# Optimization experiments

Measured on AMD Instinct MI355X. Metric: run time of the kernel, lower is better.

## Reference

```python
import jax, jax.numpy as jnp
import numpy as np

N_HEADS = 8
N_LAYERS = 2
LN_EPS = 1e-5


def _mha(x, Win, bin_, Wout, bout):
    # torch nn.MultiheadAttention, eval mode (dropout off). x: [b, s, d]
    b, s, d = x.shape
    dh = d // N_HEADS
    qkv = x @ Win.T + bin_                      # [b, s, 3d]
    q, k, v = jnp.split(qkv, 3, axis=-1)
    q = q.reshape(b, s, N_HEADS, dh)
    k = k.reshape(b, s, N_HEADS, dh)
    v = v.reshape(b, s, N_HEADS, dh)
    scores = jnp.einsum('bqhd,bkhd->bhqk', q, k) / jnp.sqrt(jnp.asarray(dh, x.dtype))
    attn = jax.nn.softmax(scores, axis=-1)
    o = jnp.einsum('bhqk,bkhd->bqhd', attn, v).reshape(b, s, d)
    return o @ Wout.T + bout


def _layer_norm(x, g, b):
    mu = jnp.mean(x, axis=-1, keepdims=True)
    var = jnp.mean(jnp.square(x - mu), axis=-1, keepdims=True)
    return (x - mu) * jax.lax.rsqrt(var + LN_EPS) * g + b


def _vertex_conv(feat, inc, prev, Win, bin_, Wout, bout, Wproj, ln_g, ln_b, alpha):
    # feat: [b,m,d], inc: [b,m,e]
    attn = _mha(feat, Win, bin_, Wout, bout)              # [b,m,d]
    scores = jnp.einsum('bme,bmd->bed', inc, attn)        # incidence aggregation
    w = jax.nn.softmax(scores, axis=1)                    # softmax over edges
    # fused form of einsum('bme,bmd->bmed') then einsum('bmed,bed->bed')
    edge = scores * w                                     # [b,e,d]
    edge = edge @ Wproj.T                                 # no-bias projection
    edge = _layer_norm(edge, ln_g, ln_b)
    if prev is not None:
        edge = alpha * prev + (1.0 - alpha) * edge
        edge = edge + prev
    return edge


def _edge_conv(inc, edge_feat, prev, Win, bin_, Wout, bout, Wproj, ln_g, ln_b, alpha):
    # inc: [b,m,e], edge_feat: [b,e,d]
    _ = _mha(edge_feat, Win, bin_, Wout, bout)            # attn computed, output unused downstream
    wef = jnp.einsum('bed,bme->bmd', edge_feat, inc)      # edge->node aggregation
    node = wef @ Wproj.T
    node = _layer_norm(node, ln_g, ln_b)
    if prev is not None:
        node = alpha * prev + (1.0 - alpha) * node
        node = node + prev
    return node


def setup_inputs() -> dict:
    key = jax.random.key(0)
    ks = jax.random.split(key, 8)
    b, m, e, d = 8, 1024, 1536, 256
    s = 0.02
    return {
        'features': jax.random.normal(ks[0], (b, m, d), jnp.float32),
        'inc_mat': (jax.random.uniform(ks[1], (b, m, e), jnp.float32) < 0.05).astype(jnp.float32),
        'vc_Win': jax.random.normal(ks[2], (3 * d, d), jnp.float32) * s,
        'vc_bin': jnp.zeros((3 * d,), jnp.float32),
        'vc_Wout': jax.random.normal(ks[3], (d, d), jnp.float32) * s,
        'vc_bout': jnp.zeros((d,), jnp.float32),
        'vc_Wproj': jax.random.normal(ks[4], (d, d), jnp.float32) * s,
        'vc_ln_g': jnp.ones((d,), jnp.float32),
        'vc_ln_b': jnp.zeros((d,), jnp.float32),
        'vc_alpha': jnp.asarray(0.5, jnp.float32),
        'ec_Win': jax.random.normal(ks[5], (3 * d, d), jnp.float32) * s,
        'ec_bin': jnp.zeros((3 * d,), jnp.float32),
        'ec_Wout': jax.random.normal(ks[6], (d, d), jnp.float32) * s,
        'ec_bout': jnp.zeros((d,), jnp.float32),
        'ec_Wproj': jax.random.normal(ks[7], (d, d), jnp.float32) * s,
        'ec_ln_g': jnp.ones((d,), jnp.float32),
        'ec_ln_b': jnp.zeros((d,), jnp.float32),
        'ec_alpha': jnp.asarray(0.5, jnp.float32),
    }


def reference(features, inc_mat,
              vc_Win, vc_bin, vc_Wout, vc_bout, vc_Wproj, vc_ln_g, vc_ln_b, vc_alpha,
              ec_Win, ec_bin, ec_Wout, ec_bout, ec_Wproj, ec_ln_g, ec_ln_b, ec_alpha):
    vc = (vc_Win, vc_bin, vc_Wout, vc_bout, vc_Wproj, vc_ln_g, vc_ln_b, vc_alpha)
    ec = (ec_Win, ec_bin, ec_Wout, ec_bout, ec_Wproj, ec_ln_g, ec_ln_b, ec_alpha)
    edge_feats = _vertex_conv(features, inc_mat, None, *vc)
    node_feats = _edge_conv(inc_mat, edge_feats, features, *ec)
    for _ in range(N_LAYERS):  # shared weights across layers, as in the torch module
        edge_feats = _vertex_conv(features, inc_mat, edge_feats, *vc)
        node_feats = _edge_conv(inc_mat, edge_feats, node_feats, *ec)
    return node_feats, edge_feats, inc_mat
```

## Files before the change

kernel.cpp:

```cpp
#include <hip/hip_runtime.h>
#include <stdint.h>


#define DEV static __device__ __forceinline__

typedef __attribute__((ext_vector_type(8))) short bf16x8;
typedef __attribute__((ext_vector_type(4))) float f32x4;

DEV uint16_t f2bf(float x){
  union{float f; uint32_t u;} v; v.f=x;
  uint32_t r = v.u + 0x7fffu + ((v.u>>16)&1u);
  return (uint16_t)(r>>16);
}
DEV float bf2f(uint16_t b){
  union{uint32_t u; float f;} v; v.u=((uint32_t)b)<<16; return v.f;
}

DEV uint32_t cvtpk_bf16(float lo, float hi){
  uint32_t d;
  asm("v_cvt_pk_bf16_f32 %0, %1, %2" : "=v"(d) : "v"(lo), "v"(hi));
  return d;
}

#if __has_builtin(__builtin_amdgcn_exp2f)
DEV float exp2fast(float x){ return __builtin_amdgcn_exp2f(x); }
#else
DEV float exp2fast(float x){ return __expf(x * 0.6931471805599453f); }
#endif

#if __has_builtin(__builtin_amdgcn_global_load_lds)
#define HAVE_GLL 1
#else
#define HAVE_GLL 0
#endif

DEV void load_lds16(const uint16_t* g, void* l){
#if HAVE_GLL
  __builtin_amdgcn_global_load_lds((const __attribute__((address_space(1))) uint32_t*)g,
                                   (__attribute__((address_space(3))) uint32_t*)l, 16, 0, 0);
#else
  *(bf16x8*)l = *(const bf16x8*)g;
#endif
}

__global__ __launch_bounds__(256)
void prep(const float* __restrict__ inc, float* __restrict__ out_inc,
          uint16_t* __restrict__ incb, uint16_t* __restrict__ incT,
          const float* __restrict__ feats, const float* __restrict__ win,
          const float* __restrict__ wout, const float* __restrict__ wpv,
          const float* __restrict__ wpe,
          uint16_t* __restrict__ xb, uint16_t* __restrict__ ow,
          uint16_t* __restrict__ oo, uint16_t* __restrict__ ov,
          uint16_t* __restrict__ oe){
  __shared__ float T[32][33];
  int bx = blockIdx.x;
  int tid = threadIdx.x;
  if (bx < 12288){
    int x = bx % 48;
    int t = bx / 48;
    int y = t % 32;
    int b = t / 32;
    int c0 = x*32, r0 = y*32;
    int tx = tid & 31, ty = tid >> 5;
    size_t base = (size_t)b*1024*1536;
#pragma unroll
    for (int j=0;j<4;++j){
      int r = r0 + ty + j*8;
      size_t idx = base + (size_t)r*1536 + c0 + tx;
      float v = inc[idx];
      T[ty+j*8][tx] = v;
      out_inc[idx] = v;
      incb[idx] = f2bf(v);
    }
    __syncthreads();
    size_t baseT = (size_t)b*1536*1024;
#pragma unroll
    for (int j=0;j<4;++j){
      int c = c0 + ty + j*8;
      incT[baseT + (size_t)c*1024 + r0 + tx] = f2bf(T[tx][ty+j*8]);
    }
  } else {
    int i = (bx - 12288)*256 + tid;
    const float* src; uint16_t* dst; int j;
    if (i < 524288){ src=feats; dst=xb; j=i; }
    else {
      i -= 524288;
      if (i < 49152){ src=win; dst=ow; j=i; }
      else if (i < 65536){ src=wout; dst=oo; j=i-49152; }
      else if (i < 81920){ src=wpv; dst=ov; j=i-65536; }
      else { src=wpe; dst=oe; j=i-81920; }
    }
    float4 v = ((const float4*)src)[j];
    union { uint16_t u[4]; uint64_t q; } p;
    p.u[0]=f2bf(v.x); p.u[1]=f2bf(v.y); p.u[2]=f2bf(v.z); p.u[3]=f2bf(v.w);
    ((uint64_t*)dst)[j] = p.q;
  }
}

template<int WM, int BK, int EPI>
__global__ __launch_bounds__(256, 3)
void gemm_nt(const uint16_t* __restrict__ A, const uint16_t* __restrict__ B,
             float* __restrict__ Cf, uint16_t* __restrict__ Cb,
             const float* __restrict__ bias,
             int M, int N, int K, long sA, long sB, long sC,
             float* __restrict__ extra){
  constexpr int AROWS = WM*32;
  constexpr int UPR = BK/8;
  constexpr int RPP = 256/UPR;
  __shared__ short As[AROWS*BK];
  __shared__ short Bs[128*BK];
  const int tid = threadIdx.x;
  const int lane = tid & 63;
  const int w = tid >> 6;
  const int wm = w & 1, wn = w >> 1;
  const int r = lane & 15, q = lane >> 4;
  const long zb = blockIdx.z;
  const uint16_t* Ab = A + zb*sA + (size_t)(blockIdx.x*AROWS)*K;
  const uint16_t* Bb = B + zb*sB + (size_t)(blockIdx.y*128)*K;
  f32x4 acc[WM][4];
#pragma unroll
  for (int i=0;i<WM;++i)
#pragma unroll
    for (int j=0;j<4;++j) acc[i][j] = (f32x4){0.f,0.f,0.f,0.f};

  const int srow = tid / UPR;
  const int sblk = tid % UPR;

  for (int kb = 0; kb < K; kb += BK){
#pragma unroll
    for (int i=0;i<AROWS/RPP;++i){
      int row = srow + RPP*i;
      int lblk = sblk ^ (row & (UPR-1));
      load_lds16(Ab + (size_t)row*K + kb + lblk*8, (char*)As + i*4096 + tid*16);
    }
#pragma unroll
    for (int i=0;i<128/RPP;++i){
      int row = srow + RPP*i;
      int lblk = sblk ^ (row & (UPR-1));
      load_lds16(Bb + (size_t)row*K + kb + lblk*8, (char*)Bs + i*4096 + tid*16);
    }
    __syncthreads();
#pragma unroll
    for (int kc=0;kc<BK/32;++kc){
      bf16x8 af[WM], bf[4];
#pragma unroll
      for (int mt=0;mt<WM;++mt){
        int m = wm*(WM*16) + mt*16 + r;
        af[mt] = *(const bf16x8*)&As[m*BK + ((kc*4 + q) ^ (m&(UPR-1)))*8];
      }
#pragma unroll
      for (int nt=0;nt<4;++nt){
        int n = wn*64 + nt*16 + r;
        bf[nt] = *(const bf16x8*)&Bs[n*BK + ((kc*4 + q) ^ (n&(UPR-1)))*8];
      }
#pragma unroll
      for (int mt=0;mt<WM;++mt)
#pragma unroll
        for (int nt=0;nt<4;++nt)
          acc[mt][nt] = __builtin_amdgcn_mfma_f32_16x16x32_bf16(af[mt], bf[nt], acc[mt][nt], 0,0,0);
    }
    __syncthreads();
  }

  const int gm0 = blockIdx.x*AROWS + wm*(WM*16);
  const int gn0 = blockIdx.y*128 + wn*64;

  if constexpr (EPI == 1){
#pragma unroll
    for (int mt=0;mt<WM;++mt){
      int gmb = gm0 + mt*16 + q*4;
      size_t bb_ = (size_t)(gmb>>10)*(256*1024);
      int mm = gmb & 1023;
#pragma unroll
      for (int nt=0;nt<4;++nt){
        int gn = gn0 + nt*16 + r;
        float bv = bias ? bias[gn] : 0.f;
        union{uint16_t u[4]; uint64_t q64;} pk;
#pragma unroll
        for (int reg=0;reg<4;++reg) pk.u[reg] = f2bf(acc[mt][nt][reg] + bv);
        *(uint64_t*)(Cb + bb_ + (size_t)gn*1024 + mm) = pk.q64;
      }
    }
  } else {
#pragma unroll
    for (int mt=0;mt<WM;++mt){
#pragma unroll
      for (int nt=0;nt<4;++nt){
        int gn = gn0 + nt*16 + r;
        float bv = bias ? bias[gn] : 0.f;
#pragma unroll
        for (int reg=0;reg<4;++reg){
          int gm = gm0 + mt*16 + q*4 + reg;
          float v = acc[mt][nt][reg] + bv;
          size_t off = (size_t)(zb*sC) + (size_t)gm*N + gn;
          if (Cf) Cf[off] = v;
          if (Cb) Cb[off] = f2bf(v);
        }
      }
    }
  }
  (void)extra;
}

__global__ __launch_bounds__(256, 4)
void gemm_score(const uint16_t* __restrict__ A,
                const uint16_t* __restrict__ B,
                float* __restrict__ part,
                uint16_t* __restrict__ VE){
  __shared__ short As[32*64];
  __shared__ short Bs[256*64];
  const int tid = threadIdx.x;
  const int lane = tid & 63;
  const int w = tid >> 6;
  const int r = lane & 15, q = lane >> 4;
  const int bx = (blockIdx.x & 7)*48 + (blockIdx.x >> 3);
  const int batch = bx / 48;
  const uint16_t* Ab = A + (size_t)bx*32*1024;
  const uint16_t* Bb = B + (size_t)batch*256*1024;

  f32x4 acc[2][4];
#pragma unroll
  for (int i=0;i<2;++i)
#pragma unroll
    for (int j=0;j<4;++j) acc[i][j] = (f32x4){0.f,0.f,0.f,0.f};

  const int srow = tid >> 3;
  const int sblk = tid & 7;

  for (int kb = 0; kb < 1024; kb += 64){
    { int lblk = sblk ^ (srow & 7);
      load_lds16(Ab + (size_t)srow*1024 + kb + lblk*8, (char*)As + tid*16); }
#pragma unroll
    for (int i=0;i<8;++i){
      int row = srow + 32*i;
      int lblk = sblk ^ (row & 7);
      load_lds16(Bb + (size_t)row*1024 + kb + lblk*8, (char*)Bs + i*4096 + tid*16);
    }
    __syncthreads();
#pragma unroll
    for (int kc=0;kc<2;++kc){
      bf16x8 af[2], bf[4];
#pragma unroll
      for (int mt=0;mt<2;++mt){
        int m = mt*16 + r;
        af[mt] = *(const bf16x8*)&As[m*64 + ((kc*4 + q) ^ (m&7))*8];
      }
#pragma unroll
      for (int nt=0;nt<4;++nt){
        int n = w*64 + nt*16 + r;
        bf[nt] = *(const bf16x8*)&Bs[n*64 + ((kc*4 + q) ^ (n&7))*8];
      }
#pragma unroll
      for (int mt=0;mt<2;++mt)
#pragma unroll
        for (int nt=0;nt<4;++nt)
          acc[mt][nt] = __builtin_amdgcn_mfma_f32_16x16x32_bf16(af[mt], bf[nt], acc[mt][nt], 0,0,0);
    }
    __syncthreads();
  }

#pragma unroll
  for (int nt=0;nt<4;++nt){
    int gn = w*64 + nt*16 + r;
    float s = 0.f;
#pragma unroll
    for (int mt=0;mt<2;++mt){
#pragma unroll
      for (int reg=0;reg<4;++reg){
        float v = acc[mt][nt][reg];
        float ev = __expf(v);
        s += ev;
        int row = mt*16 + q*4 + reg;
        VE[(size_t)(bx*32 + row)*256 + gn] = f2bf(v*ev);
      }
    }
    s += __shfl_xor(s, 16);
    s += __shfl_xor(s, 32);
    if (q == 0) part[(size_t)bx*256 + gn] = s;
  }
}

__global__ __launch_bounds__(256, 4)
void gemm_ln_edge(const uint16_t* __restrict__ SB, const uint16_t* __restrict__ B,
                  const float* __restrict__ part, const float* __restrict__ g,
                  const float* __restrict__ bb, const float* __restrict__ alpha,
                  float* __restrict__ out, uint16_t* __restrict__ baset){
  __shared__ short As[32*64];
  __shared__ short Bs[256*64];
  __shared__ float lnS[4][32], lnQ[4][32];
  __shared__ float PLinv[256];
  const int tid = threadIdx.x;
  const int lane = tid & 63;
  const int w = tid >> 6;
  const int r = lane & 15, q = lane >> 4;
  const int bx = (blockIdx.x & 7)*48 + (blockIdx.x >> 3);
  const int batch = bx / 48;

  {
    float s = 0.f;
#pragma unroll
    for (int i=0;i<48;++i) s += part[((size_t)batch*48 + i)*256 + tid];
    PLinv[tid] = 1.0f / s;
  }
  __syncthreads();

  f32x4 acc[2][4];
#pragma unroll
  for (int i=0;i<2;++i)
#pragma unroll
    for (int j=0;j<4;++j) acc[i][j] = (f32x4){0.f,0.f,0.f,0.f};

  const int srow = tid >> 3;
  const int sblk = tid & 7;

  for (int kb = 0; kb < 256; kb += 64){
    {
      bf16x8 v = *(const bf16x8*)(SB + (size_t)(bx*32 + srow)*256 + kb + sblk*8);
      const float* Lp = &PLinv[kb + sblk*8];
      float xv[8];
#pragma unroll
      for (int j=0;j<8;++j) xv[j] = bf2f((uint16_t)v[j]) * Lp[j];
      union{uint32_t u[4]; bf16x8 v8;} pk;
      pk.u[0] = cvtpk_bf16(xv[0], xv[1]);
      pk.u[1] = cvtpk_bf16(xv[2], xv[3]);
      pk.u[2] = cvtpk_bf16(xv[4], xv[5]);
      pk.u[3] = cvtpk_bf16(xv[6], xv[7]);
      *(bf16x8*)&As[srow*64 + (sblk ^ (srow&7))*8] = pk.v8;
    }
#pragma unroll
    for (int i=0;i<8;++i){
      int row = srow + 32*i;
      int lblk = sblk ^ (row & 7);
      load_lds16(B + (size_t)row*256 + kb + lblk*8, (char*)Bs + i*4096 + tid*16);
    }
    __syncthreads();
#pragma unroll
    for (int kc=0;kc<2;++kc){
      bf16x8 af[2], bf[4];
#pragma unroll
      for (int mt=0;mt<2;++mt){
        int m = mt*16 + r;
        af[mt] = *(const bf16x8*)&As[m*64 + ((kc*4 + q) ^ (m&7))*8];
      }
#pragma unroll
      for (int nt=0;nt<4;++nt){
        int n = w*64 + nt*16 + r;
        bf[nt] = *(const bf16x8*)&Bs[n*64 + ((kc*4 + q) ^ (n&7))*8];
      }
#pragma unroll
      for (int mt=0;mt<2;++mt)
#pragma unroll
        for (int nt=0;nt<4;++nt)
          acc[mt][nt] = __builtin_amdgcn_mfma_f32_16x16x32_bf16(af[mt], bf[nt], acc[mt][nt], 0,0,0);
    }
    __syncthreads();
  }

  float rs[2][4], rq[2][4];
#pragma unroll
  for (int mt=0;mt<2;++mt)
#pragma unroll
    for (int reg=0;reg<4;++reg){
      float s=0.f, s2=0.f;
#pragma unroll
      for (int nt=0;nt<4;++nt){
        float v = acc[mt][nt][reg];
        s += v; s2 += v*v;
      }
#pragma unroll
      for (int off=1; off<16; off<<=1){ s += __shfl_xor(s,off); s2 += __shfl_xor(s2,off); }
      rs[mt][reg]=s; rq[mt][reg]=s2;
    }
  if (r == 0){
#pragma unroll
    for (int mt=0;mt<2;++mt)
#pragma unroll
      for (int reg=0;reg<4;++reg){
        int row = mt*16 + q*4 + reg;
        lnS[w][row] = rs[mt][reg];
        lnQ[w][row] = rq[mt][reg];
      }
  }
  __syncthreads();

  const float c0 = 3.0f + alpha[0];
  float mu_[2][4], rstd_[2][4];
#pragma unroll
  for (int mt=0;mt<2;++mt)
#pragma unroll
    for (int reg=0;reg<4;++reg){
      int row = mt*16 + q*4 + reg;
      float S = lnS[0][row]+lnS[1][row]+lnS[2][row]+lnS[3][row];
      float Q = lnQ[0][row]+lnQ[1][row]+lnQ[2][row]+lnQ[3][row];
      float mu = S * (1.f/256.f);
      float var = fmaxf(Q*(1.f/256.f) - mu*mu, 0.f);
      mu_[mt][reg] = mu;
      rstd_[mt][reg] = rsqrtf(var + 1e-5f);
    }

  int e0 = (bx % 48) * 32;
#pragma unroll
  for (int mt=0;mt<2;++mt){
#pragma unroll
    for (int nt=0;nt<4;++nt){
      int gn = w*64 + nt*16 + r;
      float gv = g[gn], bv = bb[gn];
      union{uint16_t u[4]; uint64_t q64;} pk;
#pragma unroll
      for (int reg=0;reg<4;++reg){
        int row = mt*16 + q*4 + reg;
        size_t gm = (size_t)bx*32 + row;
        float o = ((acc[mt][nt][reg]-mu_[mt][reg])*rstd_[mt][reg]*gv + bv) * c0;
        pk.u[reg] = f2bf(o);
        out[gm*256 + gn] = o;
      }
      int ee = e0 + mt*16 + q*4;
      *(uint64_t*)(baset + ((size_t)batch*256 + gn)*1536 + ee) = pk.q64;
    }
  }
}

__global__ __launch_bounds__(256, 3)
void gemm_node_fused(const uint16_t* __restrict__ inc,
                     const uint16_t* __restrict__ baset,
                     const uint16_t* __restrict__ wpe,
                     const float* __restrict__ g, const float* __restrict__ bb,
                     const float* __restrict__ alpha,
                     const float* __restrict__ feats, float* __restrict__ out){
  __shared__ short Ws[256*64];
  __shared__ short As2[32*256];
  __shared__ short Is[32*64];
  const int tid = threadIdx.x;
  const int lane = tid & 63;
  const int w = tid >> 6;
  const int r = lane & 15, q = lane >> 4;
  const int bx = (blockIdx.x & 7)*32 + (blockIdx.x >> 3);
  const int batch = bx >> 5;
  const int mt0 = (bx & 31) * 32;

  const int srow = tid >> 3;
  const int sblk = tid & 7;

  const uint16_t* Bb = baset + (size_t)batch*256*1536;
  const uint16_t* Ib = inc + ((size_t)batch*1024 + mt0)*1536;

  f32x4 acc1[4][2];
#pragma unroll
  for (int i=0;i<4;++i)
#pragma unroll
    for (int j=0;j<2;++j) acc1[i][j] = (f32x4){0.f,0.f,0.f,0.f};

  for (int kb = 0; kb < 1536; kb += 64){
#pragma unroll
    for (int i=0;i<8;++i){
      int row = srow + 32*i;
      int lblk = sblk ^ (row & 7);
      load_lds16(Bb + (size_t)row*1536 + kb + lblk*8, (char*)Ws + i*4096 + tid*16);
    }
    { int lblk = sblk ^ (srow & 7);
      load_lds16(Ib + (size_t)srow*1536 + kb + lblk*8, (char*)Is + tid*16); }
    __syncthreads();
#pragma unroll
    for (int kc=0;kc<2;++kc){
      bf16x8 af[4], bf[2];
#pragma unroll
      for (int mt=0;mt<4;++mt){
        int d = w*64 + mt*16 + r;
        af[mt] = *(const bf16x8*)&Ws[d*64 + ((kc*4 + q) ^ (d&7))*8];
      }
#pragma unroll
      for (int nt=0;nt<2;++nt){
        int m = nt*16 + r;
        bf[nt] = *(const bf16x8*)&Is[m*64 + ((kc*4 + q) ^ (m&7))*8];
      }
#pragma unroll
      for (int mt=0;mt<4;++mt)
#pragma unroll
        for (int nt=0;nt<2;++nt)
          acc1[mt][nt] = __builtin_amdgcn_mfma_f32_16x16x32_bf16(af[mt], bf[nt], acc1[mt][nt], 0,0,0);
    }
    __syncthreads();
  }

#pragma unroll
  for (int mt=0;mt<4;++mt){
    int j = w*8 + mt*2 + (q>>1);
#pragma unroll
    for (int nt=0;nt<2;++nt){
      int m = nt*16 + r;
      union{uint16_t u[4]; uint64_t q64;} pk;
#pragma unroll
      for (int reg=0;reg<4;++reg) pk.u[reg] = f2bf(acc1[mt][nt][reg]);
      *(uint64_t*)((char*)As2 + m*512 + ((j ^ (m&7))<<4) + ((q&1)<<3)) = pk.q64;
    }
  }

  f32x4 acc2[4][2];
#pragma unroll
  for (int i=0;i<4;++i)
#pragma unroll
    for (int j=0;j<2;++j) acc2[i][j] = (f32x4){0.f,0.f,0.f,0.f};

  for (int kb = 0; kb < 256; kb += 64){
#pragma unroll
    for (int i=0;i<8;++i){
      int row = srow + 32*i;
      int lblk = sblk ^ (row & 7);
      load_lds16(wpe + (size_t)row*256 + kb + lblk*8, (char*)Ws + i*4096 + tid*16);
    }
    __syncthreads();
#pragma unroll
    for (int kc=0;kc<2;++kc){
      bf16x8 af[4], bf[2];
#pragma unroll
      for (int mt=0;mt<4;++mt){
        int dp = w*64 + mt*16 + r;
        af[mt] = *(const bf16x8*)&Ws[dp*64 + ((kc*4 + q) ^ (dp&7))*8];
      }
#pragma unroll
      for (int nt=0;nt<2;++nt){
        int m = nt*16 + r;
        int jr = (kb>>3) + kc*4 + q;
        bf[nt] = *(const bf16x8*)((char*)As2 + m*512 + ((jr ^ (m&7))<<4));
      }
#pragma unroll
      for (int mt=0;mt<4;++mt)
#pragma unroll
        for (int nt=0;nt<2;++nt)
          acc2[mt][nt] = __builtin_amdgcn_mfma_f32_16x16x32_bf16(af[mt], bf[nt], acc2[mt][nt], 0,0,0);
    }
    __syncthreads();
  }

  float* lnS = (float*)Is;
  float* lnQ = lnS + 128;
  float s_[2], q_[2];
#pragma unroll
  for (int nt=0;nt<2;++nt){
    float s=0.f, s2=0.f;
#pragma unroll
    for (int mt=0;mt<4;++mt)
#pragma unroll
      for (int reg=0;reg<4;++reg){
        float v = acc2[mt][nt][reg];
        s += v; s2 += v*v;
      }
    s += __shfl_xor(s,16); s2 += __shfl_xor(s2,16);
    s += __shfl_xor(s,32); s2 += __shfl_xor(s2,32);
    s_[nt]=s; q_[nt]=s2;
  }
  if (q == 0){
#pragma unroll
    for (int nt=0;nt<2;++nt){
      lnS[w*32 + nt*16 + r] = s_[nt];
      lnQ[w*32 + nt*16 + r] = q_[nt];
    }
  }
  __syncthreads();

  const float a = alpha[0];
  const float ap1 = 1.f + a;
  const float cn = (1.f - a)*(ap1*ap1 + ap1 + 1.f);
  const float cf = ap1*ap1*ap1;

  float mu_[2], rstd_[2];
#pragma unroll
  for (int nt=0;nt<2;++nt){
    int col = nt*16 + r;
    float S = lnS[col] + lnS[32+col] + lnS[64+col] + lnS[96+col];
    float Q = lnQ[col] + lnQ[32+col] + lnQ[64+col] + lnQ[96+col];
    float mu = S * (1.f/256.f);
    float var = fmaxf(Q*(1.f/256.f) - mu*mu, 0.f);
    mu_[nt] = mu;
    rstd_[nt] = rsqrtf(var + 1e-5f);
  }

#pragma unroll
  for (int mt=0;mt<4;++mt){
    int dp0 = w*64 + mt*16 + q*4;
    float4 gv = *(const float4*)&g[dp0];
    float4 bv = *(const float4*)&bb[dp0];
#pragma unroll
    for (int nt=0;nt<2;++nt){
      int m = nt*16 + r;
      size_t gm = (size_t)batch*1024 + mt0 + m;
      float4 fv = *(const float4*)&feats[gm*256 + dp0];
      float4 ov;
      ov.x = cf*fv.x + cn*((acc2[mt][nt][0]-mu_[nt])*rstd_[nt]*gv.x + bv.x);
      ov.y = cf*fv.y + cn*((acc2[mt][nt][1]-mu_[nt])*rstd_[nt]*gv.y + bv.y);
      ov.z = cf*fv.z + cn*((acc2[mt][nt][2]-mu_[nt])*rstd_[nt]*gv.z + bv.z);
      ov.w = cf*fv.w + cn*((acc2[mt][nt][3]-mu_[nt])*rstd_[nt]*gv.w + bv.w);
      *(float4*)&out[gm*256 + dp0] = ov;
    }
  }
}

DEV void stage_K(short* Kl, const uint16_t* __restrict__ qkv, size_t rowbase,
                 int c, int h, int kr){
  const uint16_t* kp = qkv + ((rowbase + c*256 + kr)*768 + 256 + h*32);
  int sz = (kr&3) ^ ((kr>>2)&1);
#pragma unroll
  for (int lb=0; lb<4; ++lb){
    bf16x8 v = *(const bf16x8*)(kp + lb*8);
    *(bf16x8*)&Kl[kr*32 + ((lb ^ sz))*8] = v;
  }
}

DEV void stage_V(short* VT, const uint16_t* __restrict__ qkv, size_t rowbase,
                 int c, int h, int t){
  int kvp = (t>>1)*2;
  int dhh = (t&1)*16;
  const uint16_t* v0 = qkv + ((rowbase + c*256 + kvp)*768 + 512 + h*32 + dhh);
  const uint16_t* v1 = v0 + 768;
  bf16x8 a0 = *(const bf16x8*)(v0);
  bf16x8 a1 = *(const bf16x8*)(v0+8);
  bf16x8 b0 = *(const bf16x8*)(v1);
  bf16x8 b1 = *(const bf16x8*)(v1+8);
  int blkbase = kvp>>3, off = kvp&7;
#pragma unroll
  for (int i=0;i<8;++i){
    int dh = dhh + i;
    uint32_t pack = (uint32_t)(uint16_t)a0[i] | ((uint32_t)(uint16_t)b0[i]<<16);
    *(uint32_t*)&VT[dh*256 + ((blkbase ^ (dh&7))*8) + off] = pack;
  }
#pragma unroll
  for (int i=0;i<8;++i){
    int dh = dhh + 8 + i;
    uint32_t pack = (uint32_t)(uint16_t)a1[i] | ((uint32_t)(uint16_t)b1[i]<<16);
    *(uint32_t*)&VT[dh*256 + ((blkbase ^ (dh&7))*8) + off] = pack;
  }
}

__global__ __launch_bounds__(512)
void attn_fwd(const uint16_t* __restrict__ qkv, uint16_t* __restrict__ O){
  __shared__ short Kl[256*32];
  __shared__ short VT[32*256];
  __shared__ short Pl[8][16*36];
  const int tid = threadIdx.x, lane = tid&63, w = tid>>6;
  const int r = lane&15, q = lane>>4;
  const int logical = (blockIdx.x & 7)*64 + (blockIdx.x >> 3);
  const int bh = logical >> 3, qc = logical & 7;
  const int b = bh>>3, h = bh&7;
  const int q0 = qc*128 + w*16;
  const size_t rowbase = (size_t)b*1024;

  bf16x8 aq;
  {
    const float qscale = 0.25505654380651023f;
    const uint16_t* p = qkv + ((rowbase + q0 + r)*768 + h*32 + q*8);
    bf16x8 t = *(const bf16x8*)p;
#pragma unroll
    for (int j=0;j<8;++j)
      t[j] = (short)f2bf(bf2f((uint16_t)t[j]) * qscale);
    aq = t;
  }

  f32x4 o[2];
  o[0]=(f32x4){0.f,0.f,0.f,0.f}; o[1]=(f32x4){0.f,0.f,0.f,0.f};
  float l = 0.f;

  for (int c=0;c<4;++c){
    __syncthreads();
    if (tid < 256) stage_K(Kl, qkv, rowbase, c, h, tid);
    else           stage_V(VT, qkv, rowbase, c, h, tid-256);
    __syncthreads();
    for (int s32=0; s32<8; ++s32){
#pragma unroll
      for (int t2=0;t2<2;++t2){
        int rn = s32*32 + t2*16 + r;
        int sz = (rn&3) ^ ((rn>>2)&1);
        bf16x8 bk = *(const bf16x8*)&Kl[rn*32 + ((q ^ sz))*8];
        f32x4 z = (f32x4){0.f,0.f,0.f,0.f};
        f32x4 st = __builtin_amdgcn_mfma_f32_16x16x32_bf16(bk, aq, z, 0,0,0);
        float p0 = exp2fast(st[0]);
        float p1 = exp2fast(st[1]);
        float p2 = exp2fast(st[2]);
        float p3 = exp2fast(st[3]);
        l += (p0+p1)+(p2+p3);
        union{uint32_t u[2]; uint64_t q64;} pk;
        pk.u[0] = cvtpk_bf16(p0, p1);
        pk.u[1] = cvtpk_bf16(p2, p3);
        *(uint64_t*)&Pl[w][r*36 + t2*16 + q*4] = pk.q64;
      }
      bf16x8 bv[2];
#pragma unroll
      for (int db=0;db<2;++db){
        int dh = db*16 + r;
        bv[db] = *(const bf16x8*)&VT[dh*256 + (((s32*4 + q) ^ (dh&7)))*8];
      }
      bf16x8 ap = *(const bf16x8*)&Pl[w][r*36 + q*8];
#pragma unroll
      for (int db=0;db<2;++db)
        o[db] = __builtin_amdgcn_mfma_f32_16x16x32_bf16(ap, bv[db], o[db], 0,0,0);
    }
  }

  l += __shfl_xor(l, 16);
  l += __shfl_xor(l, 32);
#pragma unroll
  for (int db=0;db<2;++db)
#pragma unroll
    for (int reg=0;reg<4;++reg){
      float li = __shfl(l, q*4 + reg);
      int qr = q0 + q*4 + reg;
      O[(rowbase + qr)*256 + h*32 + db*16 + r] = f2bf(o[db][reg] / li);
    }
}

extern "C" void kernel_launch(void* const* d_in, const int* in_sizes, int n_in,
                              void* d_out, int out_size, void* d_ws, size_t ws_size,
                              hipStream_t stream){
  const float* features = (const float*)d_in[0];
  const float* inc      = (const float*)d_in[1];
  const float* vc_Win   = (const float*)d_in[2];
  const float* vc_bin   = (const float*)d_in[3];
  const float* vc_Wout  = (const float*)d_in[4];
  const float* vc_bout  = (const float*)d_in[5];
  const float* vc_Wproj = (const float*)d_in[6];
  const float* vc_ln_g  = (const float*)d_in[7];
  const float* vc_ln_b  = (const float*)d_in[8];
  const float* vc_alpha = (const float*)d_in[9];
  const float* ec_Wproj = (const float*)d_in[14];
  const float* ec_ln_g  = (const float*)d_in[15];
  const float* ec_ln_b  = (const float*)d_in[16];
  const float* ec_alpha = (const float*)d_in[17];

  float* out = (float*)d_out;
  float* out_node = out;
  float* out_edge = out + 2097152;
  float* out_inc  = out + 5242880;

  char* ws = (char*)d_ws;
  uint16_t* XB     = (uint16_t*)(ws + 0);
  float*    PART   = (float*)   (ws + 0);
  uint16_t* WINB   = (uint16_t*)(ws + 4194304);
  uint16_t* WOUTB  = (uint16_t*)(ws + 4587520);
  uint16_t* WPVB   = (uint16_t*)(ws + 4718592);
  uint16_t* WPEB   = (uint16_t*)(ws + 4849664);
  uint16_t* INCB   = (uint16_t*)(ws + 4988928);
  uint16_t* INCT   = (uint16_t*)(ws + 30154752);
  uint16_t* QKVB   = (uint16_t*)(ws + 55320576);
  uint16_t* SCORESB= (uint16_t*)(ws + 55320576);
  uint16_t* OB     = (uint16_t*)(ws + 67903488);
  uint16_t* ATTNT  = (uint16_t*)(ws + 72097792);
  uint16_t* BASET  = (uint16_t*)(ws + 82583552);

  prep<<<14720,256,0,stream>>>(inc, out_inc, INCB, INCT,
                               features, vc_Win, vc_Wout, vc_Wproj, ec_Wproj,
                               XB, WINB, WOUTB, WPVB, WPEB);

  gemm_nt<4,64,0><<<dim3(64,6,1),256,0,stream>>>(XB, WINB, nullptr, QKVB, vc_bin,
                                                 8192,768,256, 0,0,0, nullptr);
  attn_fwd<<<512,512,0,stream>>>(QKVB, OB);
  gemm_nt<2,128,1><<<dim3(128,2,1),256,0,stream>>>(OB, WOUTB, nullptr, ATTNT, vc_bout,
                                                   8192,256,256, 0,0,0, nullptr);

  gemm_score<<<384,256,0,stream>>>(INCT, ATTNT, PART, SCORESB);

  gemm_ln_edge<<<384,256,0,stream>>>(SCORESB, WPVB, PART, vc_ln_g, vc_ln_b,
                                     vc_alpha, out_edge, BASET);

  gemm_node_fused<<<256,256,0,stream>>>(INCB, BASET, WPEB, ec_ln_g, ec_ln_b,
                                        ec_alpha, features, out_node);
}
```

Measured before the change: 256.7 us.

## Co-schedule QKV GEMM with incidence prep in one launch, add MFMA priority hints

The fp32-to-bf16 cast of features and weights moves into its own small kernel. The QKV projection GEMM is merged into a single launch with the incidence-matrix copy, cast and transpose work, so the compute-bound GEMM blocks can overlap the bandwidth-bound incidence blocks. The attention kernel also wraps its MFMA calls in s_setprio raises to favour matrix issue. Trade-offs: the merged kernel shares one LDS union sized for the GEMM, which may lower occupancy for the transpose blocks, and there is an extra launch for the cast.

```diff
diff --git a/kernel.cpp b/kernel.cpp
--- a/kernel.cpp
+++ b/kernel.cpp
@@ -44,20 +44,112 @@
 }
 
 __global__ __launch_bounds__(256)
-void prep(const float* __restrict__ inc, float* __restrict__ out_inc,
-          uint16_t* __restrict__ incb, uint16_t* __restrict__ incT,
-          const float* __restrict__ feats, const float* __restrict__ win,
-          const float* __restrict__ wout, const float* __restrict__ wpv,
-          const float* __restrict__ wpe,
-          uint16_t* __restrict__ xb, uint16_t* __restrict__ ow,
-          uint16_t* __restrict__ oo, uint16_t* __restrict__ ov,
-          uint16_t* __restrict__ oe){
-  __shared__ float T[32][33];
-  int bx = blockIdx.x;
-  int tid = threadIdx.x;
-  if (bx < 12288){
-    int x = bx % 48;
-    int t = bx / 48;
+void prep_cast(const float* __restrict__ feats, const float* __restrict__ win,
+               const float* __restrict__ wout, const float* __restrict__ wpv,
+               const float* __restrict__ wpe,
+               uint16_t* __restrict__ xb, uint16_t* __restrict__ ow,
+               uint16_t* __restrict__ oo, uint16_t* __restrict__ ov,
+               uint16_t* __restrict__ oe){
+  int i = blockIdx.x*256 + threadIdx.x;
+  const float* src; uint16_t* dst; int j;
+  if (i < 524288){ src=feats; dst=xb; j=i; }
+  else {
+    i -= 524288;
+    if (i < 49152){ src=win; dst=ow; j=i; }
+    else if (i < 65536){ src=wout; dst=oo; j=i-49152; }
+    else if (i < 81920){ src=wpv; dst=ov; j=i-65536; }
+    else { src=wpe; dst=oe; j=i-81920; }
+  }
+  float4 v = ((const float4*)src)[j];
+  union { uint16_t u[4]; uint64_t q; } p;
+  p.u[0]=f2bf(v.x); p.u[1]=f2bf(v.y); p.u[2]=f2bf(v.z); p.u[3]=f2bf(v.w);
+  ((uint64_t*)dst)[j] = p.q;
+}
+
+__global__ __launch_bounds__(256, 3)
+void qkv_incprep(const float* __restrict__ inc, float* __restrict__ out_inc,
+                 uint16_t* __restrict__ incb, uint16_t* __restrict__ incT,
+                 const uint16_t* __restrict__ A, const uint16_t* __restrict__ B,
+                 uint16_t* __restrict__ Cb, const float* __restrict__ bias){
+  __shared__ union {
+    struct { short As[128*64]; short Bs[128*64]; } g;
+    float T[32][33];
+  } sm;
+  const int tid = threadIdx.x;
+  const int bx = blockIdx.x;
+
+  if (bx < 384){
+    const int lane = tid & 63;
+    const int w = tid >> 6;
+    const int wm = w & 1, wn = w >> 1;
+    const int r = lane & 15, q = lane >> 4;
+    const int mtile = bx & 63, ntile = bx >> 6;
+    const uint16_t* Ab = A + (size_t)(mtile*128)*256;
+    const uint16_t* Bb = B + (size_t)(ntile*128)*256;
+    f32x4 acc[4][4];
+#pragma unroll
+    for (int i=0;i<4;++i)
+#pragma unroll
+      for (int j=0;j<4;++j) acc[i][j] = (f32x4){0.f,0.f,0.f,0.f};
+
+    const int srow = tid >> 3;
+    const int sblk = tid & 7;
+
+    for (int kb = 0; kb < 256; kb += 64){
+#pragma unroll
+      for (int i=0;i<4;++i){
+        int row = srow + 32*i;
+        int lblk = sblk ^ (row & 7);
+        load_lds16(Ab + (size_t)row*256 + kb + lblk*8, (char*)sm.g.As + i*4096 + tid*16);
+      }
+#pragma unroll
+      for (int i=0;i<4;++i){
+        int row = srow + 32*i;
+        int lblk = sblk ^ (row & 7);
+        load_lds16(Bb + (size_t)row*256 + kb + lblk*8, (char*)sm.g.Bs + i*4096 + tid*16);
+      }
+      __syncthreads();
+#pragma unroll
+      for (int kc=0;kc<2;++kc){
+        bf16x8 af[4], bfr[4];
+#pragma unroll
+        for (int mt=0;mt<4;++mt){
+          int m = wm*64 + mt*16 + r;
+          af[mt] = *(const bf16x8*)&sm.g.As[m*64 + ((kc*4 + q) ^ (m&7))*8];
+        }
+#pragma unroll
+        for (int nt=0;nt<4;++nt){
+          int n = wn*64 + nt*16 + r;
+          bfr[nt] = *(const bf16x8*)&sm.g.Bs[n*64 + ((kc*4 + q) ^ (n&7))*8];
+        }
+#pragma unroll
+        for (int mt=0;mt<4;++mt)
+#pragma unroll
+          for (int nt=0;nt<4;++nt)
+            acc[mt][nt] = __builtin_amdgcn_mfma_f32_16x16x32_bf16(af[mt], bfr[nt], acc[mt][nt], 0,0,0);
+      }
+      __syncthreads();
+    }
+
+    const int gm0 = mtile*128 + wm*64;
+    const int gn0 = ntile*128 + wn*64;
+#pragma unroll
+    for (int mt=0;mt<4;++mt){
+#pragma unroll
+      for (int nt=0;nt<4;++nt){
+        int gn = gn0 + nt*16 + r;
+        float bv = bias[gn];
+#pragma unroll
+        for (int reg=0;reg<4;++reg){
+          int gm = gm0 + mt*16 + q*4 + reg;
+          Cb[(size_t)gm*768 + gn] = f2bf(acc[mt][nt][reg] + bv);
+        }
+      }
+    }
+  } else {
+    int bxp = bx - 384;
+    int x = bxp % 48;
+    int t = bxp / 48;
     int y = t % 32;
     int b = t / 32;
     int c0 = x*32, r0 = y*32;
@@ -68,7 +160,7 @@
       int r = r0 + ty + j*8;
       size_t idx = base + (size_t)r*1536 + c0 + tx;
       float v = inc[idx];
-      T[ty+j*8][tx] = v;
+      sm.T[ty+j*8][tx] = v;
       out_inc[idx] = v;
       incb[idx] = f2bf(v);
     }
@@ -77,33 +169,16 @@
 #pragma unroll
     for (int j=0;j<4;++j){
       int c = c0 + ty + j*8;
-      incT[baseT + (size_t)c*1024 + r0 + tx] = f2bf(T[tx][ty+j*8]);
-    }
-  } else {
-    int i = (bx - 12288)*256 + tid;
-    const float* src; uint16_t* dst; int j;
-    if (i < 524288){ src=feats; dst=xb; j=i; }
-    else {
-      i -= 524288;
-      if (i < 49152){ src=win; dst=ow; j=i; }
-      else if (i < 65536){ src=wout; dst=oo; j=i-49152; }
-      else if (i < 81920){ src=wpv; dst=ov; j=i-65536; }
-      else { src=wpe; dst=oe; j=i-81920; }
-    }
-    float4 v = ((const float4*)src)[j];
-    union { uint16_t u[4]; uint64_t q; } p;
-    p.u[0]=f2bf(v.x); p.u[1]=f2bf(v.y); p.u[2]=f2bf(v.z); p.u[3]=f2bf(v.w);
-    ((uint64_t*)dst)[j] = p.q;
+      incT[baseT + (size_t)c*1024 + r0 + tx] = f2bf(sm.T[tx][ty+j*8]);
+    }
   }
 }
 
 template<int WM, int BK, int EPI>
 __global__ __launch_bounds__(256, 3)
 void gemm_nt(const uint16_t* __restrict__ A, const uint16_t* __restrict__ B,
-             float* __restrict__ Cf, uint16_t* __restrict__ Cb,
-             const float* __restrict__ bias,
-             int M, int N, int K, long sA, long sB, long sC,
-             float* __restrict__ extra){
+             uint16_t* __restrict__ Cb, const float* __restrict__ bias,
+             int M, int N, int K){
   constexpr int AROWS = WM*32;
   constexpr int UPR = BK/8;
   constexpr int RPP = 256/UPR;
@@ -114,9 +189,8 @@
   const int w = tid >> 6;
   const int wm = w & 1, wn = w >> 1;
   const int r = lane & 15, q = lane >> 4;
-  const long zb = blockIdx.z;
-  const uint16_t* Ab = A + zb*sA + (size_t)(blockIdx.x*AROWS)*K;
-  const uint16_t* Bb = B + zb*sB + (size_t)(blockIdx.y*128)*K;
+  const uint16_t* Ab = A + (size_t)(blockIdx.x*AROWS)*K;
+  const uint16_t* Bb = B + (size_t)(blockIdx.y*128)*K;
   f32x4 acc[WM][4];
 #pragma unroll
   for (int i=0;i<WM;++i)
@@ -142,7 +216,7 @@
     __syncthreads();
 #pragma unroll
     for (int kc=0;kc<BK/32;++kc){
-      bf16x8 af[WM], bf[4];
+      bf16x8 af[WM], bfr[4];
 #pragma unroll
       for (int mt=0;mt<WM;++mt){
         int m = wm*(WM*16) + mt*16 + r;
@@ -151,13 +225,13 @@
 #pragma unroll
       for (int nt=0;nt<4;++nt){
         int n = wn*64 + nt*16 + r;
-        bf[nt] = *(const bf16x8*)&Bs[n*BK + ((kc*4 + q) ^ (n&(UPR-1)))*8];
+        bfr[nt] = *(const bf16x8*)&Bs[n*BK + ((kc*4 + q) ^ (n&(UPR-1)))*8];
       }
 #pragma unroll
       for (int mt=0;mt<WM;++mt)
 #pragma unroll
         for (int nt=0;nt<4;++nt)
-          acc[mt][nt] = __builtin_amdgcn_mfma_f32_16x16x32_bf16(af[mt], bf[nt], acc[mt][nt], 0,0,0);
+          acc[mt][nt] = __builtin_amdgcn_mfma_f32_16x16x32_bf16(af[mt], bfr[nt], acc[mt][nt], 0,0,0);
     }
     __syncthreads();
   }
@@ -191,15 +265,11 @@
 #pragma unroll
         for (int reg=0;reg<4;++reg){
           int gm = gm0 + mt*16 + q*4 + reg;
-          float v = acc[mt][nt][reg] + bv;
-          size_t off = (size_t)(zb*sC) + (size_t)gm*N + gn;
-          if (Cf) Cf[off] = v;
-          if (Cb) Cb[off] = f2bf(v);
+          Cb[(size_t)gm*N + gn] = f2bf(acc[mt][nt][reg] + bv);
         }
       }
     }
   }
-  (void)extra;
 }
 
 __global__ __launch_bounds__(256, 4)
@@ -239,7 +309,7 @@
     __syncthreads();
 #pragma unroll
     for (int kc=0;kc<2;++kc){
-      bf16x8 af[2], bf[4];
+      bf16x8 af[2], bfr[4];
 #pragma unroll
       for (int mt=0;mt<2;++mt){
         int m = mt*16 + r;
@@ -248,13 +318,13 @@
 #pragma unroll
       for (int nt=0;nt<4;++nt){
         int n = w*64 + nt*16 + r;
-        bf[nt] = *(const bf16x8*)&Bs[n*64 + ((kc*4 + q) ^ (n&7))*8];
+        bfr[nt] = *(const bf16x8*)&Bs[n*64 + ((kc*4 + q) ^ (n&7))*8];
       }
 #pragma unroll
       for (int mt=0;mt<2;++mt)
 #pragma unroll
         for (int nt=0;nt<4;++nt)
-          acc[mt][nt] = __builtin_amdgcn_mfma_f32_16x16x32_bf16(af[mt], bf[nt], acc[mt][nt], 0,0,0);
+          acc[mt][nt] = __builtin_amdgcn_mfma_f32_16x16x32_bf16(af[mt], bfr[nt], acc[mt][nt], 0,0,0);
     }
     __syncthreads();
   }
@@ -336,7 +406,7 @@
     __syncthreads();
 #pragma unroll
     for (int kc=0;kc<2;++kc){
-      bf16x8 af[2], bf[4];
+      bf16x8 af[2], bfr[4];
 #pragma unroll
       for (int mt=0;mt<2;++mt){
         int m = mt*16 + r;
@@ -345,13 +415,13 @@
 #pragma unroll
       for (int nt=0;nt<4;++nt){
         int n = w*64 + nt*16 + r;
-        bf[nt] = *(const bf16x8*)&Bs[n*64 + ((kc*4 + q) ^ (n&7))*8];
+        bfr[nt] = *(const bf16x8*)&Bs[n*64 + ((kc*4 + q) ^ (n&7))*8];
       }
 #pragma unroll
       for (int mt=0;mt<2;++mt)
 #pragma unroll
         for (int nt=0;nt<4;++nt)
-          acc[mt][nt] = __builtin_amdgcn_mfma_f32_16x16x32_bf16(af[mt], bf[nt], acc[mt][nt], 0,0,0);
+          acc[mt][nt] = __builtin_amdgcn_mfma_f32_16x16x32_bf16(af[mt], bfr[nt], acc[mt][nt], 0,0,0);
     }
     __syncthreads();
   }
@@ -462,7 +532,7 @@
     __syncthreads();
 #pragma unroll
     for (int kc=0;kc<2;++kc){
-      bf16x8 af[4], bf[2];
+      bf16x8 af[4], bfr[2];
 #pragma unroll
       for (int mt=0;mt<4;++mt){
         int d = w*64 + mt*16 + r;
@@ -471,13 +541,13 @@
 #pragma unroll
       for (int nt=0;nt<2;++nt){
         int m = nt*16 + r;
-        bf[nt] = *(const bf16x8*)&Is[m*64 + ((kc*4 + q) ^ (m&7))*8];
+        bfr[nt] = *(const bf16x8*)&Is[m*64 + ((kc*4 + q) ^ (m&7))*8];
       }
 #pragma unroll
       for (int mt=0;mt<4;++mt)
 #pragma unroll
         for (int nt=0;nt<2;++nt)
-          acc1[mt][nt] = __builtin_amdgcn_mfma_f32_16x16x32_bf16(af[mt], bf[nt], acc1[mt][nt], 0,0,0);
+          acc1[mt][nt] = __builtin_amdgcn_mfma_f32_16x16x32_bf16(af[mt], bfr[nt], acc1[mt][nt], 0,0,0);
     }
     __syncthreads();
   }
@@ -511,7 +581,7 @@
     __syncthreads();
 #pragma unroll
     for (int kc=0;kc<2;++kc){
-      bf16x8 af[4], bf[2];
+      bf16x8 af[4], bfr[2];
 #pragma unroll
       for (int mt=0;mt<4;++mt){
         int dp = w*64 + mt*16 + r;
@@ -521,13 +591,13 @@
       for (int nt=0;nt<2;++nt){
         int m = nt*16 + r;
         int jr = (kb>>3) + kc*4 + q;
-        bf[nt] = *(const bf16x8*)((char*)As2 + m*512 + ((jr ^ (m&7))<<4));
+        bfr[nt] = *(const bf16x8*)((char*)As2 + m*512 + ((jr ^ (m&7))<<4));
       }
 #pragma unroll
       for (int mt=0;mt<4;++mt)
 #pragma unroll
         for (int nt=0;nt<2;++nt)
-          acc2[mt][nt] = __builtin_amdgcn_mfma_f32_16x16x32_bf16(af[mt], bf[nt], acc2[mt][nt], 0,0,0);
+          acc2[mt][nt] = __builtin_amdgcn_mfma_f32_16x16x32_bf16(af[mt], bfr[nt], acc2[mt][nt], 0,0,0);
     }
     __syncthreads();
   }
@@ -671,7 +741,9 @@
         int sz = (rn&3) ^ ((rn>>2)&1);
         bf16x8 bk = *(const bf16x8*)&Kl[rn*32 + ((q ^ sz))*8];
         f32x4 z = (f32x4){0.f,0.f,0.f,0.f};
+        __builtin_amdgcn_s_setprio(1);
         f32x4 st = __builtin_amdgcn_mfma_f32_16x16x32_bf16(bk, aq, z, 0,0,0);
+        __builtin_amdgcn_s_setprio(0);
         float p0 = exp2fast(st[0]);
         float p1 = exp2fast(st[1]);
         float p2 = exp2fast(st[2]);
@@ -689,9 +761,11 @@
         bv[db] = *(const bf16x8*)&VT[dh*256 + (((s32*4 + q) ^ (dh&7)))*8];
       }
       bf16x8 ap = *(const bf16x8*)&Pl[w][r*36 + q*8];
+      __builtin_amdgcn_s_setprio(1);
 #pragma unroll
       for (int db=0;db<2;++db)
         o[db] = __builtin_amdgcn_mfma_f32_16x16x32_bf16(ap, bv[db], o[db], 0,0,0);
+      __builtin_amdgcn_s_setprio(0);
     }
   }
 
@@ -745,15 +819,15 @@
   uint16_t* ATTNT  = (uint16_t*)(ws + 72097792);
   uint16_t* BASET  = (uint16_t*)(ws + 82583552);
 
-  prep<<<14720,256,0,stream>>>(inc, out_inc, INCB, INCT,
-                               features, vc_Win, vc_Wout, vc_Wproj, ec_Wproj,
-                               XB, WINB, WOUTB, WPVB, WPEB);
-
-  gemm_nt<4,64,0><<<dim3(64,6,1),256,0,stream>>>(XB, WINB, nullptr, QKVB, vc_bin,
-                                                 8192,768,256, 0,0,0, nullptr);
+  prep_cast<<<2432,256,0,stream>>>(features, vc_Win, vc_Wout, vc_Wproj, ec_Wproj,
+                                   XB, WINB, WOUTB, WPVB, WPEB);
+
+  qkv_incprep<<<12672,256,0,stream>>>(inc, out_inc, INCB, INCT,
+                                      XB, WINB, QKVB, vc_bin);
+
   attn_fwd<<<512,512,0,stream>>>(QKVB, OB);
-  gemm_nt<2,128,1><<<dim3(128,2,1),256,0,stream>>>(OB, WOUTB, nullptr, ATTNT, vc_bout,
-                                                   8192,256,256, 0,0,0, nullptr);
+  gemm_nt<2,128,1><<<dim3(128,2,1),256,0,stream>>>(OB, WOUTB, ATTNT, vc_bout,
+                                                   8192,256,256);
 
   gemm_score<<<384,256,0,stream>>>(INCT, ATTNT, PART, SCORESB);
 
```

After: 255.9 us. Within noise of the previous version (-0.3%).
